# Performance work log

Measured on AMD Instinct MI355X. Metric: run time of the kernel, lower is better.

Reference implementation:

```python
import jax, jax.numpy as jnp
import numpy as np

N_NODES = 50000
N_EDGES = 600000
D = 128


def gcn_conv(x, src, dst, W, b, n_nodes):
    """PyG GCNConv: h = D^-1/2 (A+I) D^-1/2 (x @ W) + b, messages src->dst."""
    h = x @ W  # [N, out]
    # add self loops (weight 1)
    loop = jnp.arange(n_nodes, dtype=src.dtype)
    s = jnp.concatenate([src, loop])
    d = jnp.concatenate([dst, loop])
    w = jnp.ones(s.shape[0], dtype=x.dtype)
    deg = jax.ops.segment_sum(w, d, num_segments=n_nodes)  # in-degree at target
    dinv = jnp.where(deg > 0, jax.lax.rsqrt(deg), 0.0).astype(x.dtype)
    norm = dinv[s] * w * dinv[d]  # [E+N]
    msg = h[s] * norm[:, None]  # gather + scale
    out = jax.ops.segment_sum(msg, d, num_segments=n_nodes)  # scatter-add
    return out + b


def setup_inputs() -> dict:
    key = jax.random.key(0)
    k1, k2, k3, k4, k5, k6 = jax.random.split(key, 6)
    x = jax.random.normal(k1, (N_NODES, D), dtype=jnp.float32)
    edge_index = jax.random.randint(k2, (2, N_EDGES), 0, N_NODES, dtype=jnp.int64)
    s = (1.0 / np.sqrt(D))
    W1 = jax.random.normal(k3, (D, D), dtype=jnp.float32) * s
    b1 = jnp.zeros((D,), dtype=jnp.float32)
    W2 = jax.random.normal(k4, (D, D), dtype=jnp.float32) * s
    b2 = jnp.zeros((D,), dtype=jnp.float32)
    return {"x": x, "edge_index": edge_index, "W1": W1, "b1": b1, "W2": W2, "b2": b2}


def reference(x, edge_index, W1, b1, W2, b2):
    src, dst = edge_index[0], edge_index[1]
    # two GCN layers (order=2), ReLU activation; dropout is identity at eval
    o1 = jax.nn.relu(gcn_conv(x, src, dst, W1, b1, N_NODES))
    o2 = jax.nn.relu(gcn_conv(x, src, dst, W2, b2, N_NODES))
    # combine_mode='mean'
    return 0.5 * (o1 + o2)
```

## Files before the change

kernel.cpp:

```cpp
#include <hip/hip_runtime.h>
#include <hip/hip_bf16.h>

#define N_NODES 50000
#define N_EDGES 600000
#define D 128
#define CAP 64
#define ZSTRIDE 136

typedef __attribute__((ext_vector_type(8))) short bfrag;
typedef __attribute__((ext_vector_type(4))) float ffrag;

__device__ __forceinline__ short bf16bits(float f) {
    __hip_bfloat16 h = __float2bfloat16(f);
    return *reinterpret_cast<short*>(&h);
}
__device__ __forceinline__ float bfbits2float(short b) {
    unsigned u = ((unsigned)(unsigned short)b) << 16;
    return __uint_as_float(u);
}

__device__ __forceinline__ unsigned norm_cnt(unsigned raw) {
    return raw - (raw >= 0x80000000u ? 0xAAAAAAAAu : 0u);
}

__global__ void fill_kernel(const int* __restrict__ src, const int* __restrict__ dst,
                            unsigned* __restrict__ cnt, int* __restrict__ srcs) {
    int e = blockIdx.x * 256 + threadIdx.x;
    if (e < N_EDGES) {
        int d = dst[e];
        unsigned slot = norm_cnt(atomicAdd(&cnt[d], 1u));
        if (slot < CAP) srcs[d * CAP + slot] = src[e];
    }
}

__global__ __launch_bounds__(256) void dxw_kernel(
    const float* __restrict__ x,
    const float* __restrict__ W1, const float* __restrict__ W2,
    const unsigned* __restrict__ cnt,
    __hip_bfloat162* __restrict__ xs, int* __restrict__ srcs,
    short* __restrict__ wpack)
{
    int idx = blockIdx.x * 256 + threadIdx.x;

    int node = idx >> 6;
    unsigned deg = norm_cnt(cnt[node]);
    float dv = rsqrtf((float)(deg + 1));
    float2 v = ((const float2*)x)[idx];
    __hip_bfloat162 h;
    h.x = __float2bfloat16(dv * v.x);
    h.y = __float2bfloat16(dv * v.y);
    xs[idx] = h;

    if ((idx & 63) == 0) {
        unsigned n8 = (deg + 7u) & ~7u;
        n8 = n8 < CAP ? n8 : CAP;
        for (unsigned s2 = deg; s2 < n8; ++s2) srcs[node * CAP + s2] = N_NODES;
    }

    if (idx < 64) {
        __hip_bfloat162 z0;
        z0.x = __float2bfloat16(0.f);
        z0.y = __float2bfloat16(0.f);
        xs[N_NODES * 64 + idx] = z0;
    }

    if (idx < 2 * 8 * 4 * 64 * 8) {
        int j  = idx & 7;
        int l  = (idx >> 3) & 63;
        int ks = (idx >> 9) & 3;
        int c  = (idx >> 11) & 7;
        int m  = (idx >> 14) & 1;
        int k = ks * 32 + (l >> 4) * 8 + j;
        int n = c * 16 + (l & 15);
        const float* W = m ? W2 : W1;
        wpack[idx] = bf16bits(W[k * D + n]);
    }
}

__global__ __launch_bounds__(256, 4) void fused_kernel(
    const unsigned* __restrict__ cnt,
    const int* __restrict__ srcs,
    const __hip_bfloat162* __restrict__ xs,
    const short* __restrict__ wpack,
    const float* __restrict__ b1,
    const float* __restrict__ b2,
    float* __restrict__ out)
{
    __shared__ __align__(16) short zs16[16 * ZSTRIDE];
    const int base = blockIdx.x * 16;
    const int t = threadIdx.x;
    const int lane = t & 63;
    const int g = t >> 6;
    const int p = lane & 15;
    const int q = lane >> 4;

    int sreg[4];
    unsigned n8[4];
    float dvr[4];
    bfrag vself[4];
#pragma unroll
    for (int rr = 0; rr < 4; ++rr) {
        const int node = base + g * 4 + rr;
        unsigned deg = norm_cnt(cnt[node]);
        dvr[rr] = rsqrtf((float)(deg + 1));
        unsigned m = (deg + 7u) & ~7u;
        n8[rr] = m < CAP ? m : CAP;
        sreg[rr] = srcs[node * CAP + lane];
        vself[rr] = ((const bfrag*)(xs + node * 64))[p];
    }
    unsigned mx = n8[0] > n8[1] ? n8[0] : n8[1];
    unsigned mx2 = n8[2] > n8[3] ? n8[2] : n8[3];
    mx = mx > mx2 ? mx : mx2;

    float acc[4][8];
#pragma unroll
    for (int rr = 0; rr < 4; ++rr)
#pragma unroll
        for (int j = 0; j < 8; ++j) acc[rr][j] = 0.f;

    for (unsigned e = 0; e < mx; e += 8) {
        int s0v[4], s1v[4];
#pragma unroll
        for (int rr = 0; rr < 4; ++rr) {
            int i0 = __shfl(sreg[rr], (int)e + q, 64);
            int i1 = __shfl(sreg[rr], (int)e + 4 + q, 64);
            bool act = e < n8[rr];
            i0 = i0 < 0 ? 0 : (i0 > N_NODES ? N_NODES : i0);
            i1 = i1 < 0 ? 0 : (i1 > N_NODES ? N_NODES : i1);
            s0v[rr] = act ? i0 : N_NODES;
            s1v[rr] = act ? i1 : N_NODES;
        }
        bfrag v0[4], v1[4];
#pragma unroll
        for (int rr = 0; rr < 4; ++rr) {
            v0[rr] = ((const bfrag*)(xs + s0v[rr] * 64))[p];
            v1[rr] = ((const bfrag*)(xs + s1v[rr] * 64))[p];
        }
#pragma unroll
        for (int rr = 0; rr < 4; ++rr)
#pragma unroll
            for (int j = 0; j < 8; ++j)
                acc[rr][j] += bfbits2float(v0[rr][j]) + bfbits2float(v1[rr][j]);
    }

#pragma unroll
    for (int rr = 0; rr < 4; ++rr) {
        const int r = g * 4 + rr;
#pragma unroll
        for (int j = 0; j < 8; ++j) {
            acc[rr][j] += __shfl_xor(acc[rr][j], 16, 64);
            acc[rr][j] += __shfl_xor(acc[rr][j], 32, 64);
        }
        if (q == 0) {
            bfrag zo;
#pragma unroll
            for (int j = 0; j < 8; ++j)
                zo[j] = bf16bits(dvr[rr] * (acc[rr][j] + bfbits2float(vself[rr][j])));
            *(bfrag*)&zs16[r * ZSTRIDE + p * 8] = zo;
        }
    }
    __syncthreads();

    const int m16 = lane & 15;
    const int quad = lane >> 4;
    const int c0 = 2 * g;
    const int c1 = 2 * g + 1;

    ffrag acc00 = {0.f, 0.f, 0.f, 0.f};
    ffrag acc01 = {0.f, 0.f, 0.f, 0.f};
    ffrag acc10 = {0.f, 0.f, 0.f, 0.f};
    ffrag acc11 = {0.f, 0.f, 0.f, 0.f};

#pragma unroll
    for (int ks = 0; ks < 4; ++ks) {
        bfrag a = *(const bfrag*)&zs16[m16 * ZSTRIDE + ks * 32 + quad * 8];

        bfrag b00 = *(const bfrag*)&wpack[((((0 * 8 + c0) * 4 + ks) * 64 + lane) * 8)];
        bfrag b01 = *(const bfrag*)&wpack[((((0 * 8 + c1) * 4 + ks) * 64 + lane) * 8)];
        bfrag b10 = *(const bfrag*)&wpack[((((1 * 8 + c0) * 4 + ks) * 64 + lane) * 8)];
        bfrag b11 = *(const bfrag*)&wpack[((((1 * 8 + c1) * 4 + ks) * 64 + lane) * 8)];

        acc00 = __builtin_amdgcn_mfma_f32_16x16x32_bf16(a, b00, acc00, 0, 0, 0);
        acc01 = __builtin_amdgcn_mfma_f32_16x16x32_bf16(a, b01, acc01, 0, 0, 0);
        acc10 = __builtin_amdgcn_mfma_f32_16x16x32_bf16(a, b10, acc10, 0, 0, 0);
        acc11 = __builtin_amdgcn_mfma_f32_16x16x32_bf16(a, b11, acc11, 0, 0, 0);
    }

    const int n0 = c0 * 16 + m16;
    const int n1 = c1 * 16 + m16;
    const float b1n0 = b1[n0], b1n1 = b1[n1];
    const float b2n0 = b2[n0], b2n1 = b2[n1];
#pragma unroll
    for (int reg = 0; reg < 4; ++reg) {
        int row = quad * 4 + reg;
        int node = base + row;
        float o0 = 0.5f * (fmaxf(acc00[reg] + b1n0, 0.f) + fmaxf(acc10[reg] + b2n0, 0.f));
        float o1 = 0.5f * (fmaxf(acc01[reg] + b1n1, 0.f) + fmaxf(acc11[reg] + b2n1, 0.f));
        out[node * D + n0] = o0;
        out[node * D + n1] = o1;
    }
}

extern "C" void kernel_launch(void* const* d_in, const int* in_sizes, int n_in,
                              void* d_out, int out_size, void* d_ws, size_t ws_size,
                              hipStream_t stream) {
    const float* x  = (const float*)d_in[0];
    const int*   ei = (const int*)d_in[1];
    const float* W1 = (const float*)d_in[2];
    const float* b1 = (const float*)d_in[3];
    const float* W2 = (const float*)d_in[4];
    const float* b2 = (const float*)d_in[5];
    float* out = (float*)d_out;

    const int* src = ei;
    const int* dst = ei + N_EDGES;

    char* ws = (char*)d_ws;
    unsigned* cnt  = (unsigned*)(ws + 0);
    int*      srcs = (int*)(ws + 200704);
    __hip_bfloat162* xs = (__hip_bfloat162*)(ws + 13000704);
    short*    wpack = (short*)(ws + 25800960);

    fill_kernel<<<(N_EDGES + 255) / 256, 256, 0, stream>>>(src, dst, cnt, srcs);
    dxw_kernel<<<12500, 256, 0, stream>>>(x, W1, W2, cnt, xs, srcs, wpack);
    fused_kernel<<<N_NODES / 16, 256, 0, stream>>>(cnt, srcs, xs, wpack, b1, b2, out);
}
```

Baseline: 151.6 us.

## Merge edge fill and bf16 conversion into one prep kernel, apply source norms in gather

Folds the edge-bucketing pass and the x-to-bf16 conversion into one prep kernel, so there is one fewer launch and the dependency on degree counts before scaling x goes away. Since x can no longer be prescaled by dinv[src], the fused kernel now reads cnt for each gathered source and computes rsqrt per edge, and masks unused slots by degree instead of padding srcs with a sentinel. This trades a kernel boundary for extra scattered 4-byte loads and rsqrt work in the gather loop. It also drops the prefetched self-row load in favour of a later load.

```diff
diff --git a/kernel.cpp b/kernel.cpp
--- a/kernel.cpp
+++ b/kernel.cpp
@@ -23,38 +23,25 @@
     return raw - (raw >= 0x80000000u ? 0xAAAAAAAAu : 0u);
 }
 
-__global__ void fill_kernel(const int* __restrict__ src, const int* __restrict__ dst,
-                            unsigned* __restrict__ cnt, int* __restrict__ srcs) {
-    int e = blockIdx.x * 256 + threadIdx.x;
-    if (e < N_EDGES) {
-        int d = dst[e];
-        unsigned slot = norm_cnt(atomicAdd(&cnt[d], 1u));
-        if (slot < CAP) srcs[d * CAP + slot] = src[e];
-    }
-}
-
-__global__ __launch_bounds__(256) void dxw_kernel(
-    const float* __restrict__ x,
+__global__ __launch_bounds__(256) void prep_kernel(
+    const float* __restrict__ x, const int* __restrict__ ei,
     const float* __restrict__ W1, const float* __restrict__ W2,
-    const unsigned* __restrict__ cnt,
-    __hip_bfloat162* __restrict__ xs, int* __restrict__ srcs,
-    short* __restrict__ wpack)
+    unsigned* __restrict__ cnt, int* __restrict__ srcs,
+    __hip_bfloat162* __restrict__ xs, short* __restrict__ wpack)
 {
     int idx = blockIdx.x * 256 + threadIdx.x;
 
-    int node = idx >> 6;
-    unsigned deg = norm_cnt(cnt[node]);
-    float dv = rsqrtf((float)(deg + 1));
     float2 v = ((const float2*)x)[idx];
     __hip_bfloat162 h;
-    h.x = __float2bfloat16(dv * v.x);
-    h.y = __float2bfloat16(dv * v.y);
+    h.x = __float2bfloat16(v.x);
+    h.y = __float2bfloat16(v.y);
     xs[idx] = h;
 
-    if ((idx & 63) == 0) {
-        unsigned n8 = (deg + 7u) & ~7u;
-        n8 = n8 < CAP ? n8 : CAP;
-        for (unsigned s2 = deg; s2 < n8; ++s2) srcs[node * CAP + s2] = N_NODES;
+    if (idx < N_EDGES) {
+        int s = ei[idx];
+        int d = ei[N_EDGES + idx];
+        unsigned slot = norm_cnt(atomicAdd(&cnt[d], 1u));
+        if (slot < CAP) srcs[d * CAP + slot] = s;
     }
 
     if (idx < 64) {
@@ -95,22 +82,22 @@
     const int q = lane >> 4;
 
     int sreg[4];
-    unsigned n8[4];
+    unsigned degc[4];
     float dvr[4];
-    bfrag vself[4];
 #pragma unroll
     for (int rr = 0; rr < 4; ++rr) {
         const int node = base + g * 4 + rr;
         unsigned deg = norm_cnt(cnt[node]);
         dvr[rr] = rsqrtf((float)(deg + 1));
-        unsigned m = (deg + 7u) & ~7u;
-        n8[rr] = m < CAP ? m : CAP;
+        degc[rr] = deg < CAP ? deg : CAP;
         sreg[rr] = srcs[node * CAP + lane];
-        vself[rr] = ((const bfrag*)(xs + node * 64))[p];
-    }
-    unsigned mx = n8[0] > n8[1] ? n8[0] : n8[1];
-    unsigned mx2 = n8[2] > n8[3] ? n8[2] : n8[3];
-    mx = mx > mx2 ? mx : mx2;
+    }
+    unsigned mx = 0;
+#pragma unroll
+    for (int rr = 0; rr < 4; ++rr) {
+        unsigned n8 = (degc[rr] + 7u) & ~7u;
+        mx = n8 > mx ? n8 : mx;
+    }
 
     float acc[4][8];
 #pragma unroll
@@ -119,28 +106,36 @@
         for (int j = 0; j < 8; ++j) acc[rr][j] = 0.f;
 
     for (unsigned e = 0; e < mx; e += 8) {
-        int s0v[4], s1v[4];
+        int sA[4], sB[4];
 #pragma unroll
         for (int rr = 0; rr < 4; ++rr) {
-            int i0 = __shfl(sreg[rr], (int)e + q, 64);
-            int i1 = __shfl(sreg[rr], (int)e + 4 + q, 64);
-            bool act = e < n8[rr];
-            i0 = i0 < 0 ? 0 : (i0 > N_NODES ? N_NODES : i0);
-            i1 = i1 < 0 ? 0 : (i1 > N_NODES ? N_NODES : i1);
-            s0v[rr] = act ? i0 : N_NODES;
-            s1v[rr] = act ? i1 : N_NODES;
+            int iA = __shfl(sreg[rr], (int)e + q, 64);
+            int iB = __shfl(sreg[rr], (int)e + 4 + q, 64);
+            sA[rr] = (e + (unsigned)q < degc[rr]) ? iA : N_NODES;
+            sB[rr] = (e + 4u + (unsigned)q < degc[rr]) ? iB : N_NODES;
         }
         bfrag v0[4], v1[4];
 #pragma unroll
         for (int rr = 0; rr < 4; ++rr) {
-            v0[rr] = ((const bfrag*)(xs + s0v[rr] * 64))[p];
-            v1[rr] = ((const bfrag*)(xs + s1v[rr] * 64))[p];
+            v0[rr] = ((const bfrag*)(xs + sA[rr] * 64))[p];
+            v1[rr] = ((const bfrag*)(xs + sB[rr] * 64))[p];
+        }
+        float wA[4], wB[4];
+#pragma unroll
+        for (int rr = 0; rr < 4; ++rr) {
+            unsigned cA = cnt[sA[rr]];
+            unsigned cB = cnt[sB[rr]];
+            wA[rr] = (e + (unsigned)q < degc[rr])
+                         ? rsqrtf((float)(norm_cnt(cA) + 1)) : 0.f;
+            wB[rr] = (e + 4u + (unsigned)q < degc[rr])
+                         ? rsqrtf((float)(norm_cnt(cB) + 1)) : 0.f;
         }
 #pragma unroll
         for (int rr = 0; rr < 4; ++rr)
 #pragma unroll
             for (int j = 0; j < 8; ++j)
-                acc[rr][j] += bfbits2float(v0[rr][j]) + bfbits2float(v1[rr][j]);
+                acc[rr][j] += wA[rr] * bfbits2float(v0[rr][j])
+                            + wB[rr] * bfbits2float(v1[rr][j]);
     }
 
 #pragma unroll
@@ -152,10 +147,12 @@
             acc[rr][j] += __shfl_xor(acc[rr][j], 32, 64);
         }
         if (q == 0) {
+            const int node = base + r;
+            bfrag vs = ((const bfrag*)(xs + node * 64))[p];
             bfrag zo;
 #pragma unroll
             for (int j = 0; j < 8; ++j)
-                zo[j] = bf16bits(dvr[rr] * (acc[rr][j] + bfbits2float(vself[rr][j])));
+                zo[j] = bf16bits(dvr[rr] * (acc[rr][j] + dvr[rr] * bfbits2float(vs[j])));
             *(bfrag*)&zs16[r * ZSTRIDE + p * 8] = zo;
         }
     }
@@ -212,16 +209,12 @@
     const float* b2 = (const float*)d_in[5];
     float* out = (float*)d_out;
 
-    const int* src = ei;
-    const int* dst = ei + N_EDGES;
-
     char* ws = (char*)d_ws;
     unsigned* cnt  = (unsigned*)(ws + 0);
     int*      srcs = (int*)(ws + 200704);
     __hip_bfloat162* xs = (__hip_bfloat162*)(ws + 13000704);
     short*    wpack = (short*)(ws + 25800960);
 
-    fill_kernel<<<(N_EDGES + 255) / 256, 256, 0, stream>>>(src, dst, cnt, srcs);
-    dxw_kernel<<<12500, 256, 0, stream>>>(x, W1, W2, cnt, xs, srcs, wpack);
+    prep_kernel<<<12500, 256, 0, stream>>>(x, ei, W1, W2, cnt, srcs, xs, wpack);
     fused_kernel<<<N_NODES / 16, 256, 0, stream>>>(cnt, srcs, xs, wpack, b1, b2, out);
 }
```

Result: slower. 159.1 us (+5.0%).
